# Performance work log

Measured on AMD Instinct MI355X. Metric: run time of the kernel, lower is better.

The kernel has to match this reference:

```python
import jax, jax.numpy as jnp
import numpy as np

N_PROBLEMS = 20000
N_SKILLS = 1000
EMB_SIZE = 128
TIME_LOG = 5.0
B, L = 64, 1024


def setup_inputs() -> dict:
    key = jax.random.key(0)
    ks = jax.random.split(key, 10)
    skills = jax.random.randint(ks[0], (B, L), 0, N_SKILLS)
    problems = jax.random.randint(ks[1], (B, L), 0, N_PROBLEMS)
    labels = jax.random.randint(ks[2], (B, L), 0, 2)
    times = jnp.sort(jax.random.randint(ks[3], (B, L), 0, 1_000_000), axis=-1)
    inp = jnp.stack([skills, problems, labels, times], axis=1)  # [B,4,L]
    std = 0.01
    return {
        "input": inp,
        "problem_base": std * jax.random.normal(ks[4], (N_PROBLEMS, 1), jnp.float32),
        "skill_base": std * jax.random.normal(ks[5], (N_SKILLS, 1), jnp.float32),
        "alpha_inter": std * jax.random.normal(ks[6], (N_SKILLS * 2, EMB_SIZE), jnp.float32),
        "alpha_skill": std * jax.random.normal(ks[7], (N_SKILLS, EMB_SIZE), jnp.float32),
        "beta_inter": std * jax.random.normal(ks[8], (N_SKILLS * 2, EMB_SIZE), jnp.float32),
        "beta_skill": std * jax.random.normal(ks[9], (N_SKILLS, EMB_SIZE), jnp.float32),
    }


def reference(input, problem_base, skill_base, alpha_inter, alpha_skill, beta_inter, beta_skill):
    skills = input[:, 0]    # [B,L]
    problems = input[:, 1]
    labels = input[:, 2]
    times = input[:, 3]

    mask_labels = labels * (labels < 2).astype(labels.dtype)
    inters = skills + mask_labels * N_SKILLS  # [B,L] in [0, 2*N_SKILLS)

    # pairwise Hawkes excitation / decay scores: [B,L,L]
    alphas = jnp.einsum('bie,bje->bij', alpha_inter[inters], alpha_skill[skills])
    betas = jnp.einsum('bie,bje->bij', beta_inter[inters], beta_skill[skills])
    betas = jnp.clip(betas + 1.0, 0.0, 10.0)

    dt = jnp.abs(times[:, :, None] - times[:, None, :]).astype(jnp.float32)
    log_dt = jnp.log(dt + 1e-10) / np.log(TIME_LOG)

    cross_effects = alphas * jnp.exp(-betas * log_dt)

    seq_len = skills.shape[1]
    # keep strictly-upper-triangular entries (source i before target j)
    keep = jnp.triu(jnp.ones((seq_len, seq_len), dtype=bool), k=1)
    sum_t = jnp.where(keep[None], cross_effects, 0.0).sum(axis=-2)  # [B,L]

    problem_bias = problem_base[problems][..., 0]
    skill_bias = skill_base[skills][..., 0]
    return jax.nn.sigmoid(problem_bias + skill_bias + sum_t)
```

## Files before the change

### kernel.cpp

```cpp
#include <hip/hip_runtime.h>
#include <hip/hip_bf16.h>

#define NB   64
#define SL   1024
#define EMB  128
#define NSK  1000
#define TI   64
#define NS   2

#define TB_ELEMS 768000
#define ACC_BYTE_OFF (TB_ELEMS * 2)

#define AI_B 0
#define BI_B 512000
#define AS_B 1024000
#define BS_B 1280000

using short8  = __attribute__((ext_vector_type(8))) short;
using floatx4 = __attribute__((ext_vector_type(4))) float;

#define INV_LOG2_5 0.43067655807339306f

__device__ inline unsigned cvt2(float x, float y) {
    float2 f; f.x = x; f.y = y;
    __hip_bfloat162 h = __float22bfloat162_rn(f);
    unsigned u; __builtin_memcpy(&u, &h, sizeof(u));
    return u;
}

extern "C" __global__ __launch_bounds__(256)
void cvt_tables(const float* __restrict__ ai, const float* __restrict__ bi,
                const float* __restrict__ as, const float* __restrict__ bs,
                unsigned short* __restrict__ dst)
{
    const int t = blockIdx.x * 256 + threadIdx.x;
    const long e = (long)t * 8;
    const float* src;
    if      (e < 256000) src = ai + e;
    else if (e < 512000) src = bi + (e - 256000);
    else if (e < 640000) src = as + (e - 512000);
    else                 src = bs + (e - 640000);
    float4 f0 = *(const float4*)src;
    float4 f1 = *(const float4*)(src + 4);
    uint4 pk;
    pk.x = cvt2(f0.x, f0.y); pk.y = cvt2(f0.z, f0.w);
    pk.z = cvt2(f1.x, f1.y); pk.w = cvt2(f1.z, f1.w);
    *(uint4*)(dst + e) = pk;
}

__device__ float fixup_pair(const float* __restrict__ air,
                            const float* __restrict__ bir,
                            const float* __restrict__ asr,
                            const float* __restrict__ bsr) {
    float da = 0.f, db = 0.f;
#pragma unroll 8
    for (int k = 0; k < EMB; k += 4) {
        float4 a  = *(const float4*)(air + k);
        float4 s  = *(const float4*)(asr + k);
        float4 bq = *(const float4*)(bir + k);
        float4 tt = *(const float4*)(bsr + k);
        da += a.x * s.x + a.y * s.y + a.z * s.z + a.w * s.w;
        db += bq.x * tt.x + bq.y * tt.y + bq.z * tt.z + bq.w * tt.w;
    }
    float beta = fminf(fmaxf(db + 1.f, 0.f), 10.f);
    return da * __expf(beta * 14.30676558073393f);
}

struct Stage2 { uint4 a0, a1, a2, a3, b0, b1, b2, b3; };

__device__ __forceinline__ Stage2 stage_load2(const char* __restrict__ tbc,
                                              int intr, int sq)
{
    const long ab = (long)intr * 256 + sq * 64;
    const char* pA = tbc + AI_B + ab;
    const char* pB = tbc + BI_B + ab;
    Stage2 s;
    s.a0 = *(const uint4*)(pA);      s.a1 = *(const uint4*)(pA + 16);
    s.a2 = *(const uint4*)(pA + 32); s.a3 = *(const uint4*)(pA + 48);
    s.b0 = *(const uint4*)(pB);      s.b1 = *(const uint4*)(pB + 16);
    s.b2 = *(const uint4*)(pB + 32); s.b3 = *(const uint4*)(pB + 48);
    return s;
}

__device__ __forceinline__ void stage_write2(char* buf, int srow, int wslot,
                                             const Stage2& s)
{
    char* pA = buf + srow * 256 + wslot;
    char* pAx = buf + srow * 256 + (wslot ^ 16);
    *(uint4*)(pA)        = s.a0;  *(uint4*)(pA + 128)  = s.a1;
    *(uint4*)(pAx)       = s.a2;  *(uint4*)(pAx + 128) = s.a3;
    *(uint4*)(pA + 16384)  = s.b0;  *(uint4*)(pA + 16384 + 128)  = s.b1;
    *(uint4*)(pAx + 16384) = s.b2;  *(uint4*)(pAx + 16384 + 128) = s.b3;
}

extern "C" __global__ __launch_bounds__(256, 2)
void hawkes_main(const int*   __restrict__ inp,
                 const unsigned short* __restrict__ tb,
                 float*       __restrict__ acc)
{
    __shared__ uint4 ldsq[4096];
    char* ldsc = (char*)ldsq;

    const int bid  = blockIdx.x;
    const int b    = bid & (NB - 1);
    const int r    = bid >> 6;
    const int jt   = 15 - (r >> 1);
    const int s    = r & 1;
    const int tid  = threadIdx.x;
    const int w    = tid >> 6;
    const int l    = tid & 63;
    const int quad = l >> 4;
    const int col  = l & 15;
    const int wrow = w * 16;

    const int* __restrict__ binp = inp + b * 4 * SL;
    const char* __restrict__ tbc = (const char*)tb;
    const int jbase = jt * TI;

    int tjv[4];
#pragma unroll
    for (int strip = 0; strip < 4; ++strip)
        tjv[strip] = binp[3 * SL + jbase + strip * 16 + col];

    {
        const int row  = tid >> 2;
        const int sq   = tid & 3;
        const int skj  = binp[jbase + row];
        const char* srcA = tbc + AS_B + (long)skj * 256 + sq * 64;
        const char* srcB = tbc + BS_B + (long)skj * 256 + sq * 64;
        uint4 qa[4], qb[4];
#pragma unroll
        for (int u = 0; u < 4; ++u) {
            qa[u] = *(const uint4*)(srcA + u * 16);
            qb[u] = *(const uint4*)(srcB + u * 16);
        }
        const int rx = (row & 15) << 4;
        const int wb = row * 256;
#pragma unroll
        for (int u = 0; u < 4; ++u) {
            const int slot = (((4 * sq + u) << 4) ^ rx);
            *(uint4*)(ldsc + wb + slot)         = qa[u];
            *(uint4*)(ldsc + 16384 + wb + slot) = qb[u];
        }
    }
    __syncthreads();

    short8 bfa[4][4], bfb[4][4];
#pragma unroll
    for (int strip = 0; strip < 4; ++strip) {
        const int row   = strip * 16 + col;
        const int rbase = row * 256;
        const int rx    = (row & 15) << 4;
#pragma unroll
        for (int ks = 0; ks < 4; ++ks) {
            const int cb = ((quad + ks * 4) << 4) ^ rx;
            bfa[strip][ks] = *(const short8*)(ldsc + rbase + cb);
            bfb[strip][ks] = *(const short8*)(ldsc + 16384 + rbase + cb);
        }
    }

    const int srow  = tid >> 2;
    const int sq    = tid & 3;
    const int wslot = (((2 * sq) ^ (srow & 7)) << 4);
    int intrv[8];
#pragma unroll
    for (int tt = 0; tt < 8; ++tt) {
        const int arow = (s + 2 * tt) * TI + srow;
        intrv[tt] = binp[arow] + binp[2 * SL + arow] * NSK;
    }

    int roff[4];
    {
        const int qh = quad >> 1, ql = quad & 1, c7 = col & 7;
#pragma unroll
        for (int ks = 0; ks < 4; ++ks)
            roff[ks] = (wrow + col) * 256 + ql * 128 + (((2 * ks + qh) ^ c7) << 4);
    }

    float sum[4] = {0.f, 0.f, 0.f, 0.f};

    if (s <= jt) {
        const int nt = ((jt - s) >> 1) + 1;

        Stage2 rS = stage_load2(tbc, intrv[0], sq);
        __syncthreads();
        stage_write2(ldsc, srow, wslot, rS);
        if (nt > 1) rS = stage_load2(tbc, intrv[1], sq);

#pragma unroll 1
        for (int t = 0; t < nt; ++t) {
            __syncthreads();
            const int cur = (t & 1) << 15;
            if (t + 1 < nt) stage_write2(ldsc + (cur ^ 32768), srow, wslot, rS);
            if (t + 2 < nt) rS = stage_load2(tbc, intrv[t + 2], sq);

            const int it = s + 2 * t;
            const char* bufA = ldsc + cur;
            short8 av[4], bv[4];
#pragma unroll
            for (int ks = 0; ks < 4; ++ks) {
                av[ks] = *(const short8*)(bufA + roff[ks]);
                bv[ks] = *(const short8*)(bufA + 16384 + roff[ks]);
            }
            const int4 t4 = *(const int4*)(binp + 3 * SL + it * TI + wrow + quad * 4);

            floatx4 aa[4], bb[4];
#pragma unroll
            for (int strip = 0; strip < 4; ++strip) {
                aa[strip] = floatx4{0.f, 0.f, 0.f, 0.f};
                bb[strip] = floatx4{1.f, 1.f, 1.f, 1.f};
            }
#pragma unroll
            for (int ks = 0; ks < 4; ++ks) {
#pragma unroll
                for (int strip = 0; strip < 4; ++strip) {
                    aa[strip] = __builtin_amdgcn_mfma_f32_16x16x32_bf16(av[ks], bfa[strip][ks], aa[strip], 0, 0, 0);
                    bb[strip] = __builtin_amdgcn_mfma_f32_16x16x32_bf16(bv[ks], bfb[strip][ks], bb[strip], 0, 0, 0);
                }
            }

#pragma unroll
            for (int strip = 0; strip < 4; ++strip) {
                const int tjs = tjv[strip];
#pragma unroll
                for (int rr = 0; rr < 4; ++rr) {
                    const int ti = (rr == 0) ? t4.x : (rr == 1) ? t4.y : (rr == 2) ? t4.z : t4.w;
                    const int dt = tjs - ti;
                    float lc  = __log2f((float)dt);
                    float nb  = fminf(fmaxf(bb[strip][rr], 0.f), 10.f) * (-INV_LOG2_5);
                    float arg = (dt > 0) ? nb * lc : -__builtin_inff();
                    sum[strip] += aa[strip][rr] * __builtin_amdgcn_exp2f(arg);
                }
            }
        }
    }

#pragma unroll
    for (int strip = 0; strip < 4; ++strip) {
        sum[strip] += __shfl_xor(sum[strip], 16, 64);
        sum[strip] += __shfl_xor(sum[strip], 32, 64);
    }
    __syncthreads();
    float* red = (float*)ldsc;
    red[w * 64 + quad * 16 + col] = sum[quad];
    __syncthreads();
    if (w == 0) {
        const float tot = red[l] + red[64 + l] + red[128 + l] + red[192 + l];
        acc[(((long)s * NB + b) << 10) + jbase + l] = tot;
    }
}

extern "C" __global__ __launch_bounds__(256)
void hawkes_finalize(const int* __restrict__ inp, const float* __restrict__ pbase,
                     const float* __restrict__ sbase,
                     const float* __restrict__ ai, const float* __restrict__ as,
                     const float* __restrict__ bi, const float* __restrict__ bs,
                     const float* __restrict__ acc, float* __restrict__ out)
{
    const int t = blockIdx.x * 256 + threadIdx.x;
    const int b = t >> 10, j = t & (SL - 1);
    const int* binp = inp + b * 4 * SL;
    const int tj   = binp[3 * SL + j];
    const int sk_j = binp[j];

    float corr = 0.f;
    for (int i = j - 1; i >= 0 && binp[3 * SL + i] == tj; --i) {
        const int ski = binp[i], li = binp[2 * SL + i];
        const long intr = ski + (long)li * NSK;
        corr += fixup_pair(ai + intr * EMB, bi + intr * EMB,
                           as + (long)sk_j * EMB, bs + (long)sk_j * EMB);
    }

    float sum = acc[t] + acc[NB * SL + t] + corr;
    const float x = pbase[binp[SL + j]] + sbase[sk_j] + sum;
    out[t] = 1.f / (1.f + __expf(-x));
}

extern "C" void kernel_launch(void* const* d_in, const int* in_sizes, int n_in,
                              void* d_out, int out_size, void* d_ws, size_t ws_size,
                              hipStream_t stream) {
    const int*   inp = (const int*)d_in[0];
    const float* pb  = (const float*)d_in[1];
    const float* sb  = (const float*)d_in[2];
    const float* ai  = (const float*)d_in[3];
    const float* as  = (const float*)d_in[4];
    const float* bi  = (const float*)d_in[5];
    const float* bs  = (const float*)d_in[6];

    unsigned short* tb  = (unsigned short*)d_ws;
    float*          acc = (float*)((char*)d_ws + ACC_BYTE_OFF);

    cvt_tables<<<dim3(96000 / 256), dim3(256), 0, stream>>>(ai, bi, as, bs, tb);
    hawkes_main<<<dim3(NB * 16 * NS), dim3(256), 0, stream>>>(inp, tb, acc);
    hawkes_finalize<<<dim3(NB * SL / 256), dim3(256), 0, stream>>>(
        inp, pb, sb, ai, as, bi, bs, acc, (float*)d_out);
}
```

Baseline: 116.4 us.

## Halve target tile to 32 rows, single-buffer LDS, raise occupancy to three

Each block now covers 32 target positions instead of 64, which doubles the grid and halves the per-block register and LDS footprint (32 KB, one source buffer). The launch bound asks for three blocks per CU. The double-buffered source staging becomes a single buffer with an extra barrier per iteration, and source indices are computed on the fly instead of preloaded. The aim is more resident waves and finer load balance across the triangular work. The cost is that each source tile is gathered and staged twice as often, for half as much MFMA work per load.

```diff
diff --git a/kernel.cpp b/kernel.cpp
--- a/kernel.cpp
+++ b/kernel.cpp
@@ -6,6 +6,7 @@
 #define EMB  128
 #define NSK  1000
 #define TI   64
+#define JB   32
 #define NS   2
 
 #define TB_ELEMS 768000
@@ -85,7 +86,7 @@
 __device__ __forceinline__ void stage_write2(char* buf, int srow, int wslot,
                                              const Stage2& s)
 {
-    char* pA = buf + srow * 256 + wslot;
+    char* pA  = buf + srow * 256 + wslot;
     char* pAx = buf + srow * 256 + (wslot ^ 16);
     *(uint4*)(pA)        = s.a0;  *(uint4*)(pA + 128)  = s.a1;
     *(uint4*)(pAx)       = s.a2;  *(uint4*)(pAx + 128) = s.a3;
@@ -93,19 +94,19 @@
     *(uint4*)(pAx + 16384) = s.b2;  *(uint4*)(pAx + 16384 + 128) = s.b3;
 }
 
-extern "C" __global__ __launch_bounds__(256, 2)
+extern "C" __global__ __launch_bounds__(256, 3)
 void hawkes_main(const int*   __restrict__ inp,
                  const unsigned short* __restrict__ tb,
                  float*       __restrict__ acc)
 {
-    __shared__ uint4 ldsq[4096];
+    __shared__ uint4 ldsq[2048];
     char* ldsc = (char*)ldsq;
 
     const int bid  = blockIdx.x;
     const int b    = bid & (NB - 1);
-    const int r    = bid >> 6;
-    const int jt   = 15 - (r >> 1);
-    const int s    = r & 1;
+    const int r_   = bid >> 6;
+    const int jt   = 31 - (r_ >> 1);
+    const int s    = r_ & 1;
     const int tid  = threadIdx.x;
     const int w    = tid >> 6;
     const int l    = tid & 63;
@@ -115,39 +116,34 @@
 
     const int* __restrict__ binp = inp + b * 4 * SL;
     const char* __restrict__ tbc = (const char*)tb;
-    const int jbase = jt * TI;
-
-    int tjv[4];
-#pragma unroll
-    for (int strip = 0; strip < 4; ++strip)
-        tjv[strip] = binp[3 * SL + jbase + strip * 16 + col];
+    const int jbase = jt * JB;
+
+    const int jtop = jt >> 1;
+    const int nt   = (s <= jtop) ? ((jtop - s) >> 1) + 1 : 0;
+
+    int tjv0 = binp[3 * SL + jbase + col];
+    int tjv1 = binp[3 * SL + jbase + 16 + col];
 
     {
-        const int row  = tid >> 2;
-        const int sq   = tid & 3;
-        const int skj  = binp[jbase + row];
-        const char* srcA = tbc + AS_B + (long)skj * 256 + sq * 64;
-        const char* srcB = tbc + BS_B + (long)skj * 256 + sq * 64;
-        uint4 qa[4], qb[4];
-#pragma unroll
-        for (int u = 0; u < 4; ++u) {
-            qa[u] = *(const uint4*)(srcA + u * 16);
-            qb[u] = *(const uint4*)(srcB + u * 16);
-        }
+        const int row = tid >> 3;
+        const int c2  = tid & 7;
+        const int skj = binp[jbase + row];
+        const char* srcA = tbc + AS_B + (long)skj * 256 + c2 * 32;
+        const char* srcB = tbc + BS_B + (long)skj * 256 + c2 * 32;
+        uint4 qa0 = *(const uint4*)(srcA),      qa1 = *(const uint4*)(srcA + 16);
+        uint4 qb0 = *(const uint4*)(srcB),      qb1 = *(const uint4*)(srcB + 16);
         const int rx = (row & 15) << 4;
-        const int wb = row * 256;
-#pragma unroll
-        for (int u = 0; u < 4; ++u) {
-            const int slot = (((4 * sq + u) << 4) ^ rx);
-            *(uint4*)(ldsc + wb + slot)         = qa[u];
-            *(uint4*)(ldsc + 16384 + wb + slot) = qb[u];
-        }
+        char* dst = ldsc + row * 256;
+        *(uint4*)(dst + (((2 * c2)     << 4) ^ rx)) = qa0;
+        *(uint4*)(dst + (((2 * c2 + 1) << 4) ^ rx)) = qa1;
+        *(uint4*)(dst + 8192 + (((2 * c2)     << 4) ^ rx)) = qb0;
+        *(uint4*)(dst + 8192 + (((2 * c2 + 1) << 4) ^ rx)) = qb1;
     }
     __syncthreads();
 
-    short8 bfa[4][4], bfb[4][4];
-#pragma unroll
-    for (int strip = 0; strip < 4; ++strip) {
+    short8 bfa[2][4], bfb[2][4];
+#pragma unroll
+    for (int strip = 0; strip < 2; ++strip) {
         const int row   = strip * 16 + col;
         const int rbase = row * 256;
         const int rx    = (row & 15) << 4;
@@ -155,19 +151,13 @@
         for (int ks = 0; ks < 4; ++ks) {
             const int cb = ((quad + ks * 4) << 4) ^ rx;
             bfa[strip][ks] = *(const short8*)(ldsc + rbase + cb);
-            bfb[strip][ks] = *(const short8*)(ldsc + 16384 + rbase + cb);
+            bfb[strip][ks] = *(const short8*)(ldsc + 8192 + rbase + cb);
         }
     }
 
     const int srow  = tid >> 2;
     const int sq    = tid & 3;
     const int wslot = (((2 * sq) ^ (srow & 7)) << 4);
-    int intrv[8];
-#pragma unroll
-    for (int tt = 0; tt < 8; ++tt) {
-        const int arow = (s + 2 * tt) * TI + srow;
-        intrv[tt] = binp[arow] + binp[2 * SL + arow] * NSK;
-    }
 
     int roff[4];
     {
@@ -177,75 +167,84 @@
             roff[ks] = (wrow + col) * 256 + ql * 128 + (((2 * ks + qh) ^ c7) << 4);
     }
 
-    float sum[4] = {0.f, 0.f, 0.f, 0.f};
-
-    if (s <= jt) {
-        const int nt = ((jt - s) >> 1) + 1;
-
-        Stage2 rS = stage_load2(tbc, intrv[0], sq);
+    float sum0 = 0.f, sum1 = 0.f;
+
+    if (nt > 0) {
+        Stage2 rS;
+        {
+            const int arow = s * TI + srow;
+            rS = stage_load2(tbc, binp[arow] + binp[2 * SL + arow] * NSK, sq);
+        }
         __syncthreads();
-        stage_write2(ldsc, srow, wslot, rS);
-        if (nt > 1) rS = stage_load2(tbc, intrv[1], sq);
 
 #pragma unroll 1
         for (int t = 0; t < nt; ++t) {
+            stage_write2(ldsc, srow, wslot, rS);
             __syncthreads();
-            const int cur = (t & 1) << 15;
-            if (t + 1 < nt) stage_write2(ldsc + (cur ^ 32768), srow, wslot, rS);
-            if (t + 2 < nt) rS = stage_load2(tbc, intrv[t + 2], sq);
-
-            const int it = s + 2 * t;
-            const char* bufA = ldsc + cur;
+
+            if (t + 1 < nt) {
+                const int arow = (s + 2 * (t + 1)) * TI + srow;
+                rS = stage_load2(tbc, binp[arow] + binp[2 * SL + arow] * NSK, sq);
+            }
+
+            const int itrow = (s + 2 * t) * TI;
             short8 av[4], bv[4];
 #pragma unroll
             for (int ks = 0; ks < 4; ++ks) {
-                av[ks] = *(const short8*)(bufA + roff[ks]);
-                bv[ks] = *(const short8*)(bufA + 16384 + roff[ks]);
-            }
-            const int4 t4 = *(const int4*)(binp + 3 * SL + it * TI + wrow + quad * 4);
-
-            floatx4 aa[4], bb[4];
-#pragma unroll
-            for (int strip = 0; strip < 4; ++strip) {
-                aa[strip] = floatx4{0.f, 0.f, 0.f, 0.f};
-                bb[strip] = floatx4{1.f, 1.f, 1.f, 1.f};
-            }
+                av[ks] = *(const short8*)(ldsc + roff[ks]);
+                bv[ks] = *(const short8*)(ldsc + 16384 + roff[ks]);
+            }
+            const int4 t4 = *(const int4*)(binp + 3 * SL + itrow + wrow + quad * 4);
+
+            floatx4 aa0 = {0.f,0.f,0.f,0.f}, aa1 = {0.f,0.f,0.f,0.f};
+            floatx4 bb0 = {1.f,1.f,1.f,1.f}, bb1 = {1.f,1.f,1.f,1.f};
 #pragma unroll
             for (int ks = 0; ks < 4; ++ks) {
-#pragma unroll
-                for (int strip = 0; strip < 4; ++strip) {
-                    aa[strip] = __builtin_amdgcn_mfma_f32_16x16x32_bf16(av[ks], bfa[strip][ks], aa[strip], 0, 0, 0);
-                    bb[strip] = __builtin_amdgcn_mfma_f32_16x16x32_bf16(bv[ks], bfb[strip][ks], bb[strip], 0, 0, 0);
+                aa0 = __builtin_amdgcn_mfma_f32_16x16x32_bf16(av[ks], bfa[0][ks], aa0, 0, 0, 0);
+                bb0 = __builtin_amdgcn_mfma_f32_16x16x32_bf16(bv[ks], bfb[0][ks], bb0, 0, 0, 0);
+                aa1 = __builtin_amdgcn_mfma_f32_16x16x32_bf16(av[ks], bfa[1][ks], aa1, 0, 0, 0);
+                bb1 = __builtin_amdgcn_mfma_f32_16x16x32_bf16(bv[ks], bfb[1][ks], bb1, 0, 0, 0);
+            }
+
+            __syncthreads();
+
+#pragma unroll
+            for (int rr = 0; rr < 4; ++rr) {
+                const int ti = (rr == 0) ? t4.x : (rr == 1) ? t4.y : (rr == 2) ? t4.z : t4.w;
+                {
+                    const int dt = tjv0 - ti;
+                    float lc  = __log2f((float)dt);
+                    float nb  = fminf(fmaxf(bb0[rr], 0.f), 10.f) * (-INV_LOG2_5);
+                    float arg = (dt > 0) ? nb * lc : -__builtin_inff();
+                    sum0 += aa0[rr] * __builtin_amdgcn_exp2f(arg);
                 }
-            }
-
-#pragma unroll
-            for (int strip = 0; strip < 4; ++strip) {
-                const int tjs = tjv[strip];
-#pragma unroll
-                for (int rr = 0; rr < 4; ++rr) {
-                    const int ti = (rr == 0) ? t4.x : (rr == 1) ? t4.y : (rr == 2) ? t4.z : t4.w;
-                    const int dt = tjs - ti;
+                {
+                    const int dt = tjv1 - ti;
                     float lc  = __log2f((float)dt);
-                    float nb  = fminf(fmaxf(bb[strip][rr], 0.f), 10.f) * (-INV_LOG2_5);
+                    float nb  = fminf(fmaxf(bb1[rr], 0.f), 10.f) * (-INV_LOG2_5);
                     float arg = (dt > 0) ? nb * lc : -__builtin_inff();
-                    sum[strip] += aa[strip][rr] * __builtin_amdgcn_exp2f(arg);
+                    sum1 += aa1[rr] * __builtin_amdgcn_exp2f(arg);
                 }
             }
         }
-    }
-
-#pragma unroll
-    for (int strip = 0; strip < 4; ++strip) {
-        sum[strip] += __shfl_xor(sum[strip], 16, 64);
-        sum[strip] += __shfl_xor(sum[strip], 32, 64);
-    }
+    } else {
+        __syncthreads();
+    }
+
+    sum0 += __shfl_xor(sum0, 16, 64);
+    sum0 += __shfl_xor(sum0, 32, 64);
+    sum1 += __shfl_xor(sum1, 16, 64);
+    sum1 += __shfl_xor(sum1, 32, 64);
+
     __syncthreads();
     float* red = (float*)ldsc;
-    red[w * 64 + quad * 16 + col] = sum[quad];
+    if (quad == 0) {
+        red[w * 32 + col]      = sum0;
+        red[w * 32 + 16 + col] = sum1;
+    }
     __syncthreads();
-    if (w == 0) {
-        const float tot = red[l] + red[64 + l] + red[128 + l] + red[192 + l];
+    if (w == 0 && l < JB) {
+        const float tot = red[l] + red[32 + l] + red[64 + l] + red[96 + l];
         acc[(((long)s * NB + b) << 10) + jbase + l] = tot;
     }
 }
@@ -291,7 +290,7 @@
     float*          acc = (float*)((char*)d_ws + ACC_BYTE_OFF);
 
     cvt_tables<<<dim3(96000 / 256), dim3(256), 0, stream>>>(ai, bi, as, bs, tb);
-    hawkes_main<<<dim3(NB * 16 * NS), dim3(256), 0, stream>>>(inp, tb, acc);
+    hawkes_main<<<dim3(NB * JB * NS / 1), dim3(256), 0, stream>>>(inp, tb, acc);
     hawkes_finalize<<<dim3(NB * SL / 256), dim3(256), 0, stream>>>(
         inp, pb, sb, ai, as, bi, bs, acc, (float*)d_out);
 }
```

New measurement: 121.6 us. +4.5%, slower.
